# Kernel optimization log

Hardware: AMD Instinct MI355X
Metric: run time of the kernel (lower is better)

The kernel has to match this reference:

```python
import jax, jax.numpy as jnp
import numpy as np

N_NODES = 50000
N_EDGES = 1600000
D = 64  # d_hidden // n_groups = 128 // 2
EPS = 1e-5


def setup_inputs() -> dict:
    key = jax.random.key(0)
    ks = jax.random.split(key, 6)
    x = jax.random.normal(ks[0], (N_NODES, D), dtype=jnp.float32)
    edge_index = jax.random.randint(ks[1], (2, N_EDGES), 0, N_NODES)
    dropout_mask = jax.random.uniform(ks[2], (N_NODES, D), dtype=jnp.float32)
    # LayerNorm affine params (elementwise_affine=True)
    gamma = jnp.ones((D,), jnp.float32)
    beta = jnp.zeros((D,), jnp.float32)
    # SAGEConv params: lin_l (applied to mean-aggregated neighbors, has bias),
    # lin_r (applied to root features, no bias) -- PyG defaults.
    lim = 1.0 / np.sqrt(D)
    W_l = jax.random.uniform(ks[3], (D, D), jnp.float32, -lim, lim)
    b_l = jnp.zeros((D,), jnp.float32)
    W_r = jax.random.uniform(ks[4], (D, D), jnp.float32, -lim, lim)
    return {"x": x, "dropout_mask": dropout_mask, "gamma": gamma, "beta": beta,
            "W_l": W_l, "b_l": b_l, "W_r": W_r, "edge_index": edge_index}


def reference(x, dropout_mask, gamma, beta, W_l, b_l, W_r, edge_index):
    # LayerNorm over feature dim, then ReLU, then dropout-mask multiply
    mu = jnp.mean(x, axis=-1, keepdims=True)
    var = jnp.mean((x - mu) ** 2, axis=-1, keepdims=True)
    h = (x - mu) * jax.lax.rsqrt(var + EPS) * gamma + beta  # [N, D]
    h = jax.nn.relu(h) * dropout_mask
    # SAGEConv (mean aggregation): gather source features, segment-mean by dst
    src, dst = edge_index[0], edge_index[1]
    msg = h[src]  # [E, D] edge-indexed gather
    agg = jax.ops.segment_sum(msg, dst, num_segments=N_NODES)  # [N, D]
    cnt = jax.ops.segment_sum(jnp.ones((msg.shape[0],), h.dtype), dst,
                              num_segments=N_NODES)
    agg = agg / jnp.maximum(cnt, 1.0)[:, None]  # scatter_mean (0 for isolated nodes)
    # out = lin_l(agg) + lin_r(h)
    return agg @ W_l.T + b_l + h @ W_r.T
```

## Files before the change

kernel.cpp:

```cpp
#include <hip/hip_runtime.h>

#define N_NODES 50000
#define N_EDGES 1600000
#define D 64
#define CAP 96
#define CHUNK 4096
#define NCHUNK ((N_EDGES + CHUNK - 1) / CHUNK)
#define NBUCK 196
#define DUMMY 0xFFFF
#define NROWS 65536
#define G_LNB 12500
#define G_HIST0 (G_LNB + 1)
#define G_FILL0 (G_HIST0 + NCHUNK)
#define ADJ_U4 (N_NODES * CAP * 2 / 16)
#define FILLB ((ADJ_U4 + 1023) / 1024)

typedef _Float16 f16x2 __attribute__((ext_vector_type(2)));

static __device__ __forceinline__ float dot2acc(f16x2 a, f16x2 b, float c) {
#if __has_builtin(__builtin_amdgcn_fdot2)
  return __builtin_amdgcn_fdot2(a, b, c, false);
#else
  return c + (float)a.x * (float)b.x + (float)a.y * (float)b.y;
#endif
}

static __device__ __forceinline__ f16x2 shflx2(f16x2 v, int msk) {
  return __builtin_bit_cast(
      f16x2, (unsigned)__shfl_xor((int)__builtin_bit_cast(unsigned, v), msk, 64));
}

static __device__ __forceinline__ void gpair(
    int myA, int myB, int off, int o, const char* hb, int coff,
    f16x2* aA, f16x2* aB) {
  uint4 va[4], vb[4];
#pragma unroll
  for (int j = 0; j < 4; ++j) {
    int ia = __shfl(myA, off + j * 8 + o, 64);
    va[j] = *(const uint4*)(hb + ((ia << 7) | coff));
  }
#pragma unroll
  for (int j = 0; j < 4; ++j) {
    int ib = __shfl(myB, off + j * 8 + o, 64);
    vb[j] = *(const uint4*)(hb + ((ib << 7) | coff));
  }
#pragma unroll
  for (int j = 0; j < 4; ++j) {
    aA[0] += __builtin_bit_cast(f16x2, va[j].x);
    aA[1] += __builtin_bit_cast(f16x2, va[j].y);
    aA[2] += __builtin_bit_cast(f16x2, va[j].z);
    aA[3] += __builtin_bit_cast(f16x2, va[j].w);
    aB[0] += __builtin_bit_cast(f16x2, vb[j].x);
    aB[1] += __builtin_bit_cast(f16x2, vb[j].y);
    aB[2] += __builtin_bit_cast(f16x2, vb[j].z);
    aB[3] += __builtin_bit_cast(f16x2, vb[j].w);
  }
}

__global__ __launch_bounds__(256) void k_front(
    const float* __restrict__ x, const float* __restrict__ mask,
    const float* __restrict__ gamma, const float* __restrict__ beta,
    f16x2* __restrict__ hf2, const int* __restrict__ ei,
    int* __restrict__ ghistT, uint4* __restrict__ adj4) {
  __shared__ int lhist[NBUCK];
  int b = blockIdx.x;
  if (b >= G_FILL0) {
    int base = (b - G_FILL0) * 1024;
    uint4 f;
    f.x = f.y = f.z = f.w = 0xFFFFFFFFu;
#pragma unroll
    for (int j = 0; j < 4; ++j) {
      int i = base + j * 256 + threadIdx.x;
      if (i < ADJ_U4) adj4[i] = f;
    }
    return;
  }
  if (b >= G_HIST0) {
    int base = (b - G_HIST0) * CHUNK;
    int len = min(CHUNK, N_EDGES - base);
    for (int i = threadIdx.x; i < NBUCK; i += 256) lhist[i] = 0;
    __syncthreads();
    const int4* pd = (const int4*)(ei + N_EDGES + base);
    for (int i = threadIdx.x; i < (len >> 2); i += 256) {
      int4 v = pd[i];
      atomicAdd(&lhist[((unsigned)v.x) >> 8], 1);
      atomicAdd(&lhist[((unsigned)v.y) >> 8], 1);
      atomicAdd(&lhist[((unsigned)v.z) >> 8], 1);
      atomicAdd(&lhist[((unsigned)v.w) >> 8], 1);
    }
    __syncthreads();
    for (int k = threadIdx.x; k < NBUCK; k += 256)
      ghistT[k * NCHUNK + (b - G_HIST0)] = lhist[k];
    return;
  }
  if (b == G_LNB) {
    if (threadIdx.x < 32) {
      f16x2 z;
      z.x = (_Float16)0.f;
      z.y = (_Float16)0.f;
      hf2[(size_t)DUMMY * 32 + threadIdx.x] = z;
    }
    return;
  }
  int tid = b * 256 + threadIdx.x;
  int n = tid >> 6;
  int d = tid & 63;
  float v = x[n * D + d];
  float s = v, s2 = v * v;
#pragma unroll
  for (int off = 32; off >= 1; off >>= 1) {
    s += __shfl_xor(s, off, 64);
    s2 += __shfl_xor(s2, off, 64);
  }
  float mu = s * (1.0f / D);
  float var = fmaxf(s2 * (1.0f / D) - mu * mu, 0.0f);
  float hv = (v - mu) * rsqrtf(var + 1e-5f) * gamma[d] + beta[d];
  hv = fmaxf(hv, 0.0f) * mask[n * D + d];
  float hn = __shfl_xor(hv, 1, 64);
  if ((d & 1) == 0) {
    f16x2 p;
    p.x = (_Float16)hv;
    p.y = (_Float16)hn;
    hf2[(size_t)n * 32 + (d >> 1)] = p;
  }
}

__global__ __launch_bounds__(256) void k_scan1(
    const int* __restrict__ ghistT, int* __restrict__ chunkbaseT,
    int* __restrict__ total) {
  __shared__ int sbuf[2][512];
  int k = blockIdx.x;
  int t = threadIdx.x;
  int v0 = (t < NCHUNK) ? ghistT[k * NCHUNK + t] : 0;
  int v1 = (t + 256 < NCHUNK) ? ghistT[k * NCHUNK + t + 256] : 0;
  sbuf[0][t] = v0;
  sbuf[0][t + 256] = v1;
  __syncthreads();
  int cur = 0;
#pragma unroll
  for (int off = 1; off < 512; off <<= 1) {
    int a0 = sbuf[cur][t] + ((t >= off) ? sbuf[cur][t - off] : 0);
    int a1 = sbuf[cur][t + 256] + ((t + 256 >= off) ? sbuf[cur][t + 256 - off] : 0);
    sbuf[cur ^ 1][t] = a0;
    sbuf[cur ^ 1][t + 256] = a1;
    __syncthreads();
    cur ^= 1;
  }
  if (t < NCHUNK) chunkbaseT[k * NCHUNK + t] = sbuf[cur][t] - v0;
  if (t + 256 < NCHUNK) chunkbaseT[k * NCHUNK + t + 256] = sbuf[cur][t + 256] - v1;
  if (t == 0) total[k] = sbuf[cur][NCHUNK - 1];
}

__global__ __launch_bounds__(256) void k_scan2(
    const int* __restrict__ total, int* __restrict__ bucket_start,
    const float* __restrict__ Wl, const float* __restrict__ Wr,
    f16x2* __restrict__ wf16) {
  if (blockIdx.x > 0) {
    int g = (blockIdx.x - 1) * 256 + threadIdx.x;
    float2 v = (g < 2048) ? ((const float2*)Wl)[g] : ((const float2*)Wr)[g - 2048];
    f16x2 p;
    p.x = (_Float16)v.x;
    p.y = (_Float16)v.y;
    wf16[g] = p;
    return;
  }
  __shared__ int sbuf[2][256];
  int t = threadIdx.x;
  int v = (t < NBUCK) ? total[t] : 0;
  sbuf[0][t] = v;
  __syncthreads();
  int cur = 0;
#pragma unroll
  for (int off = 1; off < 256; off <<= 1) {
    int a = sbuf[cur][t] + ((t >= off) ? sbuf[cur][t - off] : 0);
    sbuf[cur ^ 1][t] = a;
    __syncthreads();
    cur ^= 1;
  }
  if (t < NBUCK) bucket_start[t] = sbuf[cur][t] - v;
  if (t == 0) bucket_start[NBUCK] = N_EDGES;
}

__global__ __launch_bounds__(512) void k_scatter2(
    const int* __restrict__ ei, const int* __restrict__ chunkbaseT,
    const int* __restrict__ bucket_start, unsigned* __restrict__ sorted) {
  __shared__ int lcur[NBUCK];
  int b = blockIdx.x;
  int base = b * CHUNK;
  int len = min(CHUNK, N_EDGES - base);
  for (int k = threadIdx.x; k < NBUCK; k += 512)
    lcur[k] = bucket_start[k] + chunkbaseT[k * NCHUNK + b];
  __syncthreads();
  const int4* ps = (const int4*)(ei + base);
  const int4* pd = (const int4*)(ei + N_EDGES + base);
  for (int i = threadIdx.x; i < (len >> 2); i += 512) {
    int4 s4 = ps[i];
    int4 d4 = pd[i];
    {
      unsigned dst = (unsigned)d4.x, src = (unsigned)s4.x;
      int pos = atomicAdd(&lcur[dst >> 8], 1);
      sorted[pos] = (dst << 16) | src;
    }
    {
      unsigned dst = (unsigned)d4.y, src = (unsigned)s4.y;
      int pos = atomicAdd(&lcur[dst >> 8], 1);
      sorted[pos] = (dst << 16) | src;
    }
    {
      unsigned dst = (unsigned)d4.z, src = (unsigned)s4.z;
      int pos = atomicAdd(&lcur[dst >> 8], 1);
      sorted[pos] = (dst << 16) | src;
    }
    {
      unsigned dst = (unsigned)d4.w, src = (unsigned)s4.w;
      int pos = atomicAdd(&lcur[dst >> 8], 1);
      sorted[pos] = (dst << 16) | src;
    }
  }
}

__global__ __launch_bounds__(1024) void k_place3(
    const unsigned* __restrict__ sorted, const int* __restrict__ bucket_start,
    unsigned short* __restrict__ adj, float* __restrict__ invd) {
  __shared__ int lcnt[256];
  int k = blockIdx.x;
  if (threadIdx.x < 256) lcnt[threadIdx.x] = 0;
  __syncthreads();
  int s = bucket_start[k];
  int e = bucket_start[k + 1];
  for (int i = s + threadIdx.x; i < e; i += 1024) {
    unsigned rec = sorted[i];
    int dst = (int)(rec >> 16);
    int pos = atomicAdd(&lcnt[dst & 255], 1);
    if (pos < CAP) adj[(size_t)dst * CAP + pos] = (unsigned short)(rec & 0xffffu);
  }
  __syncthreads();
  if (threadIdx.x < 256) {
    int dst = (k << 8) + threadIdx.x;
    if (dst < N_NODES)
      invd[dst] = 1.0f / (float)max(min(lcnt[threadIdx.x], CAP), 1);
  }
}

__global__ __launch_bounds__(512, 6) void k_gather_out(
    const f16x2* __restrict__ hf2, const float* __restrict__ invd,
    const unsigned short* __restrict__ adj, const f16x2* __restrict__ wf16,
    const float* __restrict__ bl, float* __restrict__ out) {
  __shared__ f16x2 sWl2[D][34];
  __shared__ f16x2 sWr2[D][34];
  __shared__ f16x2 sA2[16][32];
  __shared__ f16x2 sH2[16][32];
  int w = threadIdx.x >> 6;
  int L = threadIdx.x & 63;
  {
    int i0 = threadIdx.x * 4;
    int row = i0 >> 5, col = i0 & 31;
    const f16x2* wl = wf16;
    const f16x2* wr = wf16 + 2048;
#pragma unroll
    for (int j = 0; j < 4; ++j) {
      sWl2[row][col + j] = wl[i0 + j];
      sWr2[row][col + j] = wr[i0 + j];
    }
  }
  __syncthreads();

  int nA = blockIdx.x * 16 + w * 2;
  int nB = nA + 1;
  int abA = nA * CAP, abB = nB * CAP;
  int myA = (int)__builtin_nontemporal_load(adj + abA + L);
  int myB = (int)__builtin_nontemporal_load(adj + abB + L);
  float invA = __builtin_nontemporal_load(invd + nA);
  float invB = __builtin_nontemporal_load(invd + nB);

  unsigned long long bm =
      __ballot(myA != DUMMY) | __ballot(myB != DUMMY);

  int o = L >> 3;
  int c8 = L & 7;
  int coff = c8 << 4;
  const char* hb = (const char*)hf2;

  f16x2 aA[4], aB[4];
#pragma unroll
  for (int t = 0; t < 4; ++t) {
    aA[t] = __builtin_bit_cast(f16x2, 0u);
    aB[t] = __builtin_bit_cast(f16x2, 0u);
  }
  gpair(myA, myB, 0, o, hb, coff, aA, aB);
  if ((bm >> 32) != 0ull) gpair(myA, myB, 32, o, hb, coff, aA, aB);
  if ((bm >> 63) != 0ull) {
    int myA2 = (L < 32) ? (int)__builtin_nontemporal_load(adj + abA + 64 + L)
                        : DUMMY;
    int myB2 = (L < 32) ? (int)__builtin_nontemporal_load(adj + abB + 64 + L)
                        : DUMMY;
    gpair(myA2, myB2, 0, o, hb, coff, aA, aB);
  }

#pragma unroll
  for (int msk = 8; msk <= 32; msk <<= 1) {
#pragma unroll
    for (int t = 0; t < 4; ++t) {
      aA[t] += shflx2(aA[t], msk);
      aB[t] += shflx2(aB[t], msk);
    }
  }
  if (o == 0) {
#pragma unroll
    for (int t = 0; t < 4; ++t) {
      f16x2 p;
      p.x = (_Float16)((float)aA[t].x * invA);
      p.y = (_Float16)((float)aA[t].y * invA);
      sA2[2 * w][4 * c8 + t] = p;
    }
  } else if (o == 1) {
#pragma unroll
    for (int t = 0; t < 4; ++t) {
      f16x2 p;
      p.x = (_Float16)((float)aB[t].x * invB);
      p.y = (_Float16)((float)aB[t].y * invB);
      sA2[2 * w + 1][4 * c8 + t] = p;
    }
  }
  if (L < 32) sH2[2 * w][L] = hf2[(size_t)nA * 32 + L];
  else sH2[2 * w + 1][L - 32] = hf2[(size_t)nB * 32 + (L - 32)];

  float accA = bl[L];
  float accB = accA;
#pragma unroll
  for (int k2 = 0; k2 < 32; ++k2) {
    f16x2 wlv = sWl2[L][k2];
    f16x2 wrv = sWr2[L][k2];
    accA = dot2acc(sA2[2 * w][k2], wlv, accA);
    accA = dot2acc(sH2[2 * w][k2], wrv, accA);
    accB = dot2acc(sA2[2 * w + 1][k2], wlv, accB);
    accB = dot2acc(sH2[2 * w + 1][k2], wrv, accB);
  }
  __builtin_nontemporal_store(accA, out + (size_t)nA * D + L);
  __builtin_nontemporal_store(accB, out + (size_t)nB * D + L);
}

extern "C" void kernel_launch(void* const* d_in, const int* in_sizes, int n_in,
                              void* d_out, int out_size, void* d_ws,
                              size_t ws_size, hipStream_t stream) {
  const float* x = (const float*)d_in[0];
  const float* mask = (const float*)d_in[1];
  const float* gamma = (const float*)d_in[2];
  const float* beta = (const float*)d_in[3];
  const float* Wl = (const float*)d_in[4];
  const float* bl = (const float*)d_in[5];
  const float* Wr = (const float*)d_in[6];
  const int* ei = (const int*)d_in[7];
  float* out = (float*)d_out;

  f16x2* hf2 = (f16x2*)d_ws;
  unsigned* sorted = (unsigned*)(hf2 + (size_t)NROWS * 32);
  int* ghistT = (int*)(sorted + (size_t)N_EDGES);
  int* chunkbaseT = ghistT + NBUCK * NCHUNK;
  int* total = chunkbaseT + NBUCK * NCHUNK;
  int* bucket_start = total + NBUCK;
  float* invd = (float*)(bucket_start + (NBUCK + 2));
  unsigned short* adj = (unsigned short*)(invd + N_NODES);
  f16x2* wf16 = (f16x2*)(adj + (size_t)N_NODES * CAP);

  dim3 blk(256);
  k_front<<<G_FILL0 + FILLB, blk, 0, stream>>>(x, mask, gamma, beta, hf2, ei,
                                               ghistT, (uint4*)adj);
  k_scan1<<<NBUCK, blk, 0, stream>>>(ghistT, chunkbaseT, total);
  k_scan2<<<17, blk, 0, stream>>>(total, bucket_start, Wl, Wr, wf16);
  k_scatter2<<<NCHUNK, dim3(512), 0, stream>>>(ei, chunkbaseT, bucket_start,
                                               sorted);
  k_place3<<<NBUCK, dim3(1024), 0, stream>>>(sorted, bucket_start, adj, invd);
  k_gather_out<<<N_NODES / 16, dim3(512), 0, stream>>>(hf2, invd, adj, wf16,
                                                       bl, out);
}
```

Before: 75.09 us.

## Replace per-chunk histogram scans with atomic bucket offsets and targeted adjacency padding

Per-chunk histograms and the two-level scan are replaced by global atomic bucket totals, a single-block scan, and per-block atomic reservation of bucket ranges during scatter. Scatter records are staged in shared memory so the edge list is read once. The full adjacency fill with DUMMY is removed; instead place3 pads only the slots the gather will read (up to 64 or 96 per node pair). The gather now issues all 64 first-tier loads unconditionally with occupancy hint lowered to 5, trading fewer launches and less memory traffic for atomic contention and nondeterministic edge order within buckets.

```diff
diff --git a/kernel.cpp b/kernel.cpp
--- a/kernel.cpp
+++ b/kernel.cpp
@@ -11,9 +11,8 @@
 #define NROWS 65536
 #define G_LNB 12500
 #define G_HIST0 (G_LNB + 1)
-#define G_FILL0 (G_HIST0 + NCHUNK)
-#define ADJ_U4 (N_NODES * CAP * 2 / 16)
-#define FILLB ((ADJ_U4 + 1023) / 1024)
+#define G_W0 (G_HIST0 + NCHUNK)
+#define G_FRONT (G_W0 + 16)
 
 typedef _Float16 f16x2 __attribute__((ext_vector_type(2)));
 
@@ -30,30 +29,59 @@
       f16x2, (unsigned)__shfl_xor((int)__builtin_bit_cast(unsigned, v), msk, 64));
 }
 
-static __device__ __forceinline__ void gpair(
-    int myA, int myB, int off, int o, const char* hb, int coff,
-    f16x2* aA, f16x2* aB) {
+static __device__ __forceinline__ f16x2 bc2(unsigned u) {
+  return __builtin_bit_cast(f16x2, u);
+}
+
+static __device__ __forceinline__ void g64(
+    int myA, int myB, int o, const char* hb, int coff, f16x2* aA, f16x2* aB) {
+  uint4 va[8], vb[8];
+#pragma unroll
+  for (int j = 0; j < 8; ++j) {
+    int ia = __shfl(myA, j * 8 + o, 64);
+    va[j] = *(const uint4*)(hb + ((ia << 7) | coff));
+  }
+#pragma unroll
+  for (int j = 0; j < 8; ++j) {
+    int ib = __shfl(myB, j * 8 + o, 64);
+    vb[j] = *(const uint4*)(hb + ((ib << 7) | coff));
+  }
+#pragma unroll
+  for (int j = 0; j < 8; ++j) {
+    aA[0] += bc2(va[j].x);
+    aA[1] += bc2(va[j].y);
+    aA[2] += bc2(va[j].z);
+    aA[3] += bc2(va[j].w);
+    aB[0] += bc2(vb[j].x);
+    aB[1] += bc2(vb[j].y);
+    aB[2] += bc2(vb[j].z);
+    aB[3] += bc2(vb[j].w);
+  }
+}
+
+static __device__ __forceinline__ void g32(
+    int myA, int myB, int o, const char* hb, int coff, f16x2* aA, f16x2* aB) {
   uint4 va[4], vb[4];
 #pragma unroll
   for (int j = 0; j < 4; ++j) {
-    int ia = __shfl(myA, off + j * 8 + o, 64);
+    int ia = __shfl(myA, j * 8 + o, 64);
     va[j] = *(const uint4*)(hb + ((ia << 7) | coff));
   }
 #pragma unroll
   for (int j = 0; j < 4; ++j) {
-    int ib = __shfl(myB, off + j * 8 + o, 64);
+    int ib = __shfl(myB, j * 8 + o, 64);
     vb[j] = *(const uint4*)(hb + ((ib << 7) | coff));
   }
 #pragma unroll
   for (int j = 0; j < 4; ++j) {
-    aA[0] += __builtin_bit_cast(f16x2, va[j].x);
-    aA[1] += __builtin_bit_cast(f16x2, va[j].y);
-    aA[2] += __builtin_bit_cast(f16x2, va[j].z);
-    aA[3] += __builtin_bit_cast(f16x2, va[j].w);
-    aB[0] += __builtin_bit_cast(f16x2, vb[j].x);
-    aB[1] += __builtin_bit_cast(f16x2, vb[j].y);
-    aB[2] += __builtin_bit_cast(f16x2, vb[j].z);
-    aB[3] += __builtin_bit_cast(f16x2, vb[j].w);
+    aA[0] += bc2(va[j].x);
+    aA[1] += bc2(va[j].y);
+    aA[2] += bc2(va[j].z);
+    aA[3] += bc2(va[j].w);
+    aB[0] += bc2(vb[j].x);
+    aB[1] += bc2(vb[j].y);
+    aB[2] += bc2(vb[j].z);
+    aB[3] += bc2(vb[j].w);
   }
 }
 
@@ -61,18 +89,17 @@
     const float* __restrict__ x, const float* __restrict__ mask,
     const float* __restrict__ gamma, const float* __restrict__ beta,
     f16x2* __restrict__ hf2, const int* __restrict__ ei,
-    int* __restrict__ ghistT, uint4* __restrict__ adj4) {
+    int* __restrict__ gtot, const float* __restrict__ Wl,
+    const float* __restrict__ Wr, f16x2* __restrict__ wf16) {
   __shared__ int lhist[NBUCK];
   int b = blockIdx.x;
-  if (b >= G_FILL0) {
-    int base = (b - G_FILL0) * 1024;
-    uint4 f;
-    f.x = f.y = f.z = f.w = 0xFFFFFFFFu;
-#pragma unroll
-    for (int j = 0; j < 4; ++j) {
-      int i = base + j * 256 + threadIdx.x;
-      if (i < ADJ_U4) adj4[i] = f;
-    }
+  if (b >= G_W0) {
+    int g = (b - G_W0) * 256 + threadIdx.x;
+    float2 v = (g < 2048) ? ((const float2*)Wl)[g] : ((const float2*)Wr)[g - 2048];
+    f16x2 p;
+    p.x = (_Float16)v.x;
+    p.y = (_Float16)v.y;
+    wf16[g] = p;
     return;
   }
   if (b >= G_HIST0) {
@@ -90,7 +117,7 @@
     }
     __syncthreads();
     for (int k = threadIdx.x; k < NBUCK; k += 256)
-      ghistT[k * NCHUNK + (b - G_HIST0)] = lhist[k];
+      if (lhist[k]) atomicAdd(&gtot[k], lhist[k]);
     return;
   }
   if (b == G_LNB) {
@@ -125,48 +152,12 @@
   }
 }
 
-__global__ __launch_bounds__(256) void k_scan1(
-    const int* __restrict__ ghistT, int* __restrict__ chunkbaseT,
-    int* __restrict__ total) {
-  __shared__ int sbuf[2][512];
-  int k = blockIdx.x;
-  int t = threadIdx.x;
-  int v0 = (t < NCHUNK) ? ghistT[k * NCHUNK + t] : 0;
-  int v1 = (t + 256 < NCHUNK) ? ghistT[k * NCHUNK + t + 256] : 0;
-  sbuf[0][t] = v0;
-  sbuf[0][t + 256] = v1;
-  __syncthreads();
-  int cur = 0;
-#pragma unroll
-  for (int off = 1; off < 512; off <<= 1) {
-    int a0 = sbuf[cur][t] + ((t >= off) ? sbuf[cur][t - off] : 0);
-    int a1 = sbuf[cur][t + 256] + ((t + 256 >= off) ? sbuf[cur][t + 256 - off] : 0);
-    sbuf[cur ^ 1][t] = a0;
-    sbuf[cur ^ 1][t + 256] = a1;
-    __syncthreads();
-    cur ^= 1;
-  }
-  if (t < NCHUNK) chunkbaseT[k * NCHUNK + t] = sbuf[cur][t] - v0;
-  if (t + 256 < NCHUNK) chunkbaseT[k * NCHUNK + t + 256] = sbuf[cur][t + 256] - v1;
-  if (t == 0) total[k] = sbuf[cur][NCHUNK - 1];
-}
-
-__global__ __launch_bounds__(256) void k_scan2(
-    const int* __restrict__ total, int* __restrict__ bucket_start,
-    const float* __restrict__ Wl, const float* __restrict__ Wr,
-    f16x2* __restrict__ wf16) {
-  if (blockIdx.x > 0) {
-    int g = (blockIdx.x - 1) * 256 + threadIdx.x;
-    float2 v = (g < 2048) ? ((const float2*)Wl)[g] : ((const float2*)Wr)[g - 2048];
-    f16x2 p;
-    p.x = (_Float16)v.x;
-    p.y = (_Float16)v.y;
-    wf16[g] = p;
-    return;
-  }
+__global__ __launch_bounds__(256) void k_scan(
+    const int* __restrict__ gtot, int* __restrict__ bucket_start,
+    int* __restrict__ gcur) {
   __shared__ int sbuf[2][256];
   int t = threadIdx.x;
-  int v = (t < NBUCK) ? total[t] : 0;
+  int v = (t < NBUCK) ? gtot[t] : 0;
   sbuf[0][t] = v;
   __syncthreads();
   int cur = 0;
@@ -177,45 +168,48 @@
     __syncthreads();
     cur ^= 1;
   }
-  if (t < NBUCK) bucket_start[t] = sbuf[cur][t] - v;
+  if (t < NBUCK) {
+    int s = sbuf[cur][t] - v;
+    bucket_start[t] = s;
+    gcur[t] = s;
+  }
   if (t == 0) bucket_start[NBUCK] = N_EDGES;
 }
 
 __global__ __launch_bounds__(512) void k_scatter2(
-    const int* __restrict__ ei, const int* __restrict__ chunkbaseT,
-    const int* __restrict__ bucket_start, unsigned* __restrict__ sorted) {
+    const int* __restrict__ ei, int* __restrict__ gcur,
+    unsigned* __restrict__ sorted) {
+  __shared__ unsigned srec[CHUNK];
+  __shared__ int lhist[NBUCK];
   __shared__ int lcur[NBUCK];
   int b = blockIdx.x;
   int base = b * CHUNK;
   int len = min(CHUNK, N_EDGES - base);
-  for (int k = threadIdx.x; k < NBUCK; k += 512)
-    lcur[k] = bucket_start[k] + chunkbaseT[k * NCHUNK + b];
+  int q = len >> 2;
+  for (int k = threadIdx.x; k < NBUCK; k += 512) lhist[k] = 0;
   __syncthreads();
   const int4* ps = (const int4*)(ei + base);
   const int4* pd = (const int4*)(ei + N_EDGES + base);
-  for (int i = threadIdx.x; i < (len >> 2); i += 512) {
+  for (int i = threadIdx.x; i < q; i += 512) {
     int4 s4 = ps[i];
     int4 d4 = pd[i];
-    {
-      unsigned dst = (unsigned)d4.x, src = (unsigned)s4.x;
-      int pos = atomicAdd(&lcur[dst >> 8], 1);
-      sorted[pos] = (dst << 16) | src;
-    }
-    {
-      unsigned dst = (unsigned)d4.y, src = (unsigned)s4.y;
-      int pos = atomicAdd(&lcur[dst >> 8], 1);
-      sorted[pos] = (dst << 16) | src;
-    }
-    {
-      unsigned dst = (unsigned)d4.z, src = (unsigned)s4.z;
-      int pos = atomicAdd(&lcur[dst >> 8], 1);
-      sorted[pos] = (dst << 16) | src;
-    }
-    {
-      unsigned dst = (unsigned)d4.w, src = (unsigned)s4.w;
-      int pos = atomicAdd(&lcur[dst >> 8], 1);
-      sorted[pos] = (dst << 16) | src;
-    }
+    srec[0 * q + i] = (((unsigned)d4.x) << 16) | (unsigned)s4.x;
+    srec[1 * q + i] = (((unsigned)d4.y) << 16) | (unsigned)s4.y;
+    srec[2 * q + i] = (((unsigned)d4.z) << 16) | (unsigned)s4.z;
+    srec[3 * q + i] = (((unsigned)d4.w) << 16) | (unsigned)s4.w;
+    atomicAdd(&lhist[((unsigned)d4.x) >> 8], 1);
+    atomicAdd(&lhist[((unsigned)d4.y) >> 8], 1);
+    atomicAdd(&lhist[((unsigned)d4.z) >> 8], 1);
+    atomicAdd(&lhist[((unsigned)d4.w) >> 8], 1);
+  }
+  __syncthreads();
+  for (int k = threadIdx.x; k < NBUCK; k += 512)
+    lcur[k] = lhist[k] ? atomicAdd(&gcur[k], lhist[k]) : 0;
+  __syncthreads();
+  for (int i = threadIdx.x; i < len; i += 512) {
+    unsigned rec = srec[i];
+    int pos = atomicAdd(&lcur[rec >> 24], 1);
+    sorted[pos] = rec;
   }
 }
 
@@ -223,6 +217,8 @@
     const unsigned* __restrict__ sorted, const int* __restrict__ bucket_start,
     unsigned short* __restrict__ adj, float* __restrict__ invd) {
   __shared__ int lcnt[256];
+  __shared__ int sown[256];
+  __shared__ int send[256];
   int k = blockIdx.x;
   if (threadIdx.x < 256) lcnt[threadIdx.x] = 0;
   __syncthreads();
@@ -235,14 +231,27 @@
     if (pos < CAP) adj[(size_t)dst * CAP + pos] = (unsigned short)(rec & 0xffffu);
   }
   __syncthreads();
+  if (threadIdx.x < 256) sown[threadIdx.x] = min(lcnt[threadIdx.x], CAP);
+  __syncthreads();
   if (threadIdx.x < 256) {
-    int dst = (k << 8) + threadIdx.x;
-    if (dst < N_NODES)
-      invd[dst] = 1.0f / (float)max(min(lcnt[threadIdx.x], CAP), 1);
-  }
-}
-
-__global__ __launch_bounds__(512, 6) void k_gather_out(
+    int t = threadIdx.x;
+    int own = sown[t];
+    int par = sown[t ^ 1];
+    send[t] = (max(own, par) >= 64) ? 96 : 64;
+    int dst = (k << 8) + t;
+    if (dst < N_NODES) invd[dst] = 1.0f / (float)max(own, 1);
+  }
+  __syncthreads();
+  for (int idx = threadIdx.x; idx < 256 * 96; idx += 1024) {
+    int dl = idx / 96;
+    int slot = idx - dl * 96;
+    int dst = (k << 8) + dl;
+    if (dst < N_NODES && slot >= sown[dl] && slot < send[dl])
+      adj[(size_t)dst * CAP + slot] = (unsigned short)DUMMY;
+  }
+}
+
+__global__ __launch_bounds__(512, 5) void k_gather_out(
     const f16x2* __restrict__ hf2, const float* __restrict__ invd,
     const unsigned short* __restrict__ adj, const f16x2* __restrict__ wf16,
     const float* __restrict__ bl, float* __restrict__ out) {
@@ -273,8 +282,7 @@
   float invA = __builtin_nontemporal_load(invd + nA);
   float invB = __builtin_nontemporal_load(invd + nB);
 
-  unsigned long long bm =
-      __ballot(myA != DUMMY) | __ballot(myB != DUMMY);
+  unsigned long long bm = __ballot(myA != DUMMY) | __ballot(myB != DUMMY);
 
   int o = L >> 3;
   int c8 = L & 7;
@@ -284,17 +292,16 @@
   f16x2 aA[4], aB[4];
 #pragma unroll
   for (int t = 0; t < 4; ++t) {
-    aA[t] = __builtin_bit_cast(f16x2, 0u);
-    aB[t] = __builtin_bit_cast(f16x2, 0u);
-  }
-  gpair(myA, myB, 0, o, hb, coff, aA, aB);
-  if ((bm >> 32) != 0ull) gpair(myA, myB, 32, o, hb, coff, aA, aB);
+    aA[t] = bc2(0u);
+    aB[t] = bc2(0u);
+  }
+  g64(myA, myB, o, hb, coff, aA, aB);
   if ((bm >> 63) != 0ull) {
     int myA2 = (L < 32) ? (int)__builtin_nontemporal_load(adj + abA + 64 + L)
                         : DUMMY;
     int myB2 = (L < 32) ? (int)__builtin_nontemporal_load(adj + abB + 64 + L)
                         : DUMMY;
-    gpair(myA2, myB2, 0, o, hb, coff, aA, aB);
+    g32(myA2, myB2, o, hb, coff, aA, aB);
   }
 
 #pragma unroll
@@ -355,21 +362,20 @@
 
   f16x2* hf2 = (f16x2*)d_ws;
   unsigned* sorted = (unsigned*)(hf2 + (size_t)NROWS * 32);
-  int* ghistT = (int*)(sorted + (size_t)N_EDGES);
-  int* chunkbaseT = ghistT + NBUCK * NCHUNK;
-  int* total = chunkbaseT + NBUCK * NCHUNK;
-  int* bucket_start = total + NBUCK;
-  float* invd = (float*)(bucket_start + (NBUCK + 2));
-  unsigned short* adj = (unsigned short*)(invd + N_NODES);
-  f16x2* wf16 = (f16x2*)(adj + (size_t)N_NODES * CAP);
+  unsigned short* adj = (unsigned short*)(sorted + N_EDGES);
+  float* invd = (float*)(adj + (size_t)N_NODES * CAP);
+  f16x2* wf16 = (f16x2*)(invd + N_NODES);
+  int* gtot = (int*)(wf16 + 4096);
+  int* bucket_start = gtot + NBUCK;
+  int* gcur = bucket_start + 200;
+
+  hipMemsetAsync(gtot, 0, NBUCK * sizeof(int), stream);
 
   dim3 blk(256);
-  k_front<<<G_FILL0 + FILLB, blk, 0, stream>>>(x, mask, gamma, beta, hf2, ei,
-                                               ghistT, (uint4*)adj);
-  k_scan1<<<NBUCK, blk, 0, stream>>>(ghistT, chunkbaseT, total);
-  k_scan2<<<17, blk, 0, stream>>>(total, bucket_start, Wl, Wr, wf16);
-  k_scatter2<<<NCHUNK, dim3(512), 0, stream>>>(ei, chunkbaseT, bucket_start,
-                                               sorted);
+  k_front<<<G_FRONT, blk, 0, stream>>>(x, mask, gamma, beta, hf2, ei, gtot,
+                                       Wl, Wr, wf16);
+  k_scan<<<1, blk, 0, stream>>>(gtot, bucket_start, gcur);
+  k_scatter2<<<NCHUNK, dim3(512), 0, stream>>>(ei, gcur, sorted);
   k_place3<<<NBUCK, dim3(1024), 0, stream>>>(sorted, bucket_start, adj, invd);
   k_gather_out<<<N_NODES / 16, dim3(512), 0, stream>>>(hf2, invd, adj, wf16,
                                                        bl, out);
```

Result: slower. 96.26 us (+28.2%).
